# Kernel tuning notes

Measured on AMD Instinct MI355X. Metric: run time of the kernel, lower is better.

Reference implementation:

```python
import jax, jax.numpy as jnp
import numpy as np

B, H, V, T = 32768, 1024, 9, 20
EOS = 8

def setup_inputs() -> dict:
    key = jax.random.key(0)
    ks = jax.random.split(key, 10)
    s_fc = 1.0 / np.sqrt(784)
    s_ih = 1.0 / np.sqrt(V)
    s_hh = 1.0 / np.sqrt(H)
    u = jax.random.uniform(ks[9], (T, B, V), jnp.float32, 1e-10, 1.0)
    return {
        "x": jax.random.normal(ks[0], (B, 784), jnp.float32),
        "tau": jnp.float32(1.0),
        "fc_w": jax.random.normal(ks[1], (H, 784), jnp.float32) * s_fc,
        "w_ih": jax.random.normal(ks[2], (3 * H, V), jnp.float32) * s_ih,
        "w_hh": jax.random.normal(ks[3], (3 * H, H), jnp.float32) * s_hh,
        "b_ih": jax.random.normal(ks[4], (3 * H,), jnp.float32) * s_hh,
        "b_hh": jax.random.normal(ks[5], (3 * H,), jnp.float32) * s_hh,
        "proj_w": jax.random.normal(ks[6], (V, H), jnp.float32) * s_hh,
        "proj_b": jax.random.normal(ks[7], (V,), jnp.float32) * s_hh,
        # standard Gumbel(0,1) noise, precomputed for all T steps
        "gumbel": -jnp.log(-jnp.log(u)),
    }


def reference(x, tau, fc_w, w_ih, w_hh, b_ih, b_hh, proj_w, proj_b, gumbel):
    # context = gelu(fc(x)); dropout is identity (eval mode)
    h0 = jax.nn.gelu(x @ fc_w.T, approximate=False)  # [B, H]
    b = x.shape[0]
    tok0 = jnp.zeros((b, V), x.dtype).at[:, 0].set(1.0)  # BOS one-hot

    def step(carry, g):
        h, tok, finished, lengths, t = carry
        gi = tok @ w_ih.T + b_ih            # [B, 3H]
        gh = h @ w_hh.T + b_hh              # [B, 3H]
        i_r, i_z, i_n = jnp.split(gi, 3, axis=-1)
        h_r, h_z, h_n = jnp.split(gh, 3, axis=-1)
        r = jax.nn.sigmoid(i_r + h_r)
        z = jax.nn.sigmoid(i_z + h_z)
        n = jnp.tanh(i_n + r * h_n)
        h_new = (1.0 - z) * n + z * h
        logits = h_new @ proj_w.T + proj_b  # [B, V]
        y_soft = jax.nn.softmax((logits + g) / tau, axis=-1)
        idx = jnp.argmax(y_soft, axis=-1)
        y_hard = jax.nn.one_hot(idx, V, dtype=y_soft.dtype)
        y = y_hard + y_soft - jax.lax.stop_gradient(y_soft)  # straight-through
        newly = (idx == EOS) & (~finished)
        lengths = jnp.where(newly, t + 1, lengths)
        finished = finished | newly
        return (h_new, y, finished, lengths, t + 1), y

    carry0 = (h0, tok0,
              jnp.zeros((b,), jnp.bool_),
              jnp.full((b,), T, jnp.int32),
              jnp.int32(0))
    (_, _, _, lengths, _), toks = jax.lax.scan(step, carry0, gumbel)
    message = jnp.transpose(toks, (1, 0, 2))  # [B, T, V]
    return message, lengths
```

## Files before the change

### kernel.cpp

```cpp
#include <hip/hip_runtime.h>
#include <math.h>

#define Bsz 32768
#define Hd  1024
#define Vn  9
#define Tn  20
#define EOSv 8
#define KFC 784

typedef float f4 __attribute__((ext_vector_type(4)));
typedef float f32x16 __attribute__((ext_vector_type(16)));
typedef _Float16 h8 __attribute__((ext_vector_type(8)));
typedef unsigned short us4 __attribute__((ext_vector_type(4)));
typedef unsigned short us8v __attribute__((ext_vector_type(8)));

__device__ __forceinline__ unsigned short f16_rne(float x) {
    _Float16 h = (_Float16)x;
    return __builtin_bit_cast(unsigned short, h);
}
__device__ __forceinline__ float f16_val(unsigned short u) {
    return (float)__builtin_bit_cast(_Float16, u);
}
__device__ __forceinline__ void split2h(float x, unsigned short& p0, unsigned short& p1) {
    p0 = f16_rne(x);
    float r = x - f16_val(p0);
    p1 = f16_rne(r);
}

__global__ __launch_bounds__(256) void k_init(int* __restrict__ st,
                                              float* __restrict__ lenf) {
    int i = blockIdx.x * 256 + threadIdx.x;
    if (i < Bsz) { st[i] = 0; lenf[i] = (float)Tn; }
}

__global__ __launch_bounds__(256) void k_prep(const float* __restrict__ wih,
                                              const float* __restrict__ bih,
                                              float* __restrict__ giTab) {
    int i = blockIdx.x * 256 + threadIdx.x;
    int tk = i / 3072, n = i - tk * 3072;
    giTab[i] = wih[(size_t)n * Vn + tk] + bih[n];
}

__global__ __launch_bounds__(256) void k_prepB(const float* __restrict__ whh,
                                               unsigned short* __restrict__ wp) {
    int g = blockIdx.x * 256 + threadIdx.x;
    int lane = g & 63, u = g >> 6;
    int p = u & 1, kc = (u >> 1) & 63, ct = u >> 7;
    int col = ct * 32 + (lane & 31);
    int k = kc * 16 + (lane >> 5) * 8;
    const float* src = whh + (size_t)col * Hd + k;
    unsigned short v[8];
    #pragma unroll
    for (int i = 0; i < 8; ++i) {
        unsigned short s0, s1; split2h(src[i], s0, s1);
        v[i] = (p == 0) ? s0 : s1;
    }
    unsigned short* dst = wp + (size_t)u * 512 + lane * 8;
    us4 w0; w0[0]=v[0]; w0[1]=v[1]; w0[2]=v[2]; w0[3]=v[3];
    us4 w1; w1[0]=v[4]; w1[1]=v[5]; w1[2]=v[6]; w1[3]=v[7];
    *(us4*)dst = w0;
    *(us4*)(dst + 4) = w1;
}

__global__ __launch_bounds__(256) void k_fcP(const float* __restrict__ x,
                                             const float* __restrict__ fcw,
                                             float* __restrict__ h0,
                                             unsigned short* __restrict__ ap) {
    __shared__ float As[16][68];
    __shared__ float Ws[16][68];
    const int tid = threadIdx.x;
    const int tx = tid & 15, ty = tid >> 4;
    const int m0 = blockIdx.x * 64, n0 = blockIdx.y * 64;
    const int lrow = tid >> 2, lkc = (tid & 3) << 2;
    float acc[4][4] = {};
    for (int k0 = 0; k0 < KFC; k0 += 16) {
        f4 a = *(const f4*)(x   + (size_t)(m0 + lrow) * KFC + k0 + lkc);
        f4 w = *(const f4*)(fcw + (size_t)(n0 + lrow) * KFC + k0 + lkc);
        #pragma unroll
        for (int q = 0; q < 4; ++q) { As[lkc + q][lrow] = a[q]; Ws[lkc + q][lrow] = w[q]; }
        __syncthreads();
        #pragma unroll
        for (int kk = 0; kk < 16; ++kk) {
            f4 av = *(const f4*)&As[kk][ty * 4];
            f4 wv = *(const f4*)&Ws[kk][tx * 4];
            #pragma unroll
            for (int i = 0; i < 4; ++i)
                #pragma unroll
                for (int j = 0; j < 4; ++j)
                    acc[i][j] = fmaf(av[i], wv[j], acc[i][j]);
        }
        __syncthreads();
    }
    #pragma unroll
    for (int i = 0; i < 4; ++i) {
        const int row = m0 + ty * 4 + i;
        const int cb = n0 + tx * 4;
        f4 hv;
        us4 q0, q1;
        #pragma unroll
        for (int j = 0; j < 4; ++j) {
            float v = acc[i][j];
            float gl = 0.5f * v * (1.0f + erff(v * 0.70710678118654752f));
            hv[j] = gl;
            unsigned short s0, s1; split2h(gl, s0, s1);
            q0[j] = s0; q1[j] = s1;
        }
        *(f4*)&h0[(size_t)row * Hd + cb] = hv;
        const size_t ub = ((size_t)(row >> 5) * 64 + (cb >> 4)) * 2;
        const int slot = (row & 31) + ((cb >> 3) & 1) * 32;
        const int eo = (tx & 1) * 4;
        *(us4*)&ap[(ub + 0) * 512 + slot * 8 + eo] = q0;
        *(us4*)&ap[(ub + 1) * 512 + slot * 8 + eo] = q1;
    }
}

__global__ __launch_bounds__(256, 2) void k_step(
        const unsigned short* __restrict__ ap, float* __restrict__ h,
        const unsigned short* __restrict__ wp, const float* __restrict__ bhh,
        const float* __restrict__ giTab, const int* __restrict__ st) {
    const int tid = threadIdx.x;
    const int lane = tid & 63, wid = tid >> 6;
    const int wm = wid >> 1, wn = wid & 1;
    const int l31 = lane & 31, lh = lane >> 5;

    const int w = blockIdx.x;
    const int cg = (w & 7) * 2 + ((w >> 3) & 1);
    const int rb = w >> 4;
    const int m_blk = rb * 128;
    const int c0 = cg * 64;

    f32x16 acc[2][3];
    #pragma unroll
    for (int mt = 0; mt < 2; ++mt)
        #pragma unroll
        for (int g = 0; g < 3; ++g)
            #pragma unroll
            for (int e = 0; e < 16; ++e) acc[mt][g][e] = 0.0f;

    const unsigned short* ab[2][2];
    #pragma unroll
    for (int mt = 0; mt < 2; ++mt)
        #pragma unroll
        for (int p = 0; p < 2; ++p)
            ab[mt][p] = ap + ((size_t)(rb * 4 + wm * 2 + mt) * 64 * 2 + p) * 512 + lane * 8;
    const unsigned short* bb[3][2];
    #pragma unroll
    for (int g = 0; g < 3; ++g)
        #pragma unroll
        for (int p = 0; p < 2; ++p)
            bb[g][p] = wp + ((size_t)(g * 32 + cg * 2 + wn) * 64 * 2 + p) * 512 + lane * 8;

    h8 A0[2][2], A1[2][2], B0[3][2], B1[3][2];

    auto load = [&](int s, h8 (&A)[2][2], h8 (&B)[3][2]) {
        const size_t off = (size_t)s * 1024;
        #pragma unroll
        for (int mt = 0; mt < 2; ++mt)
            #pragma unroll
            for (int p = 0; p < 2; ++p)
                A[mt][p] = *(const h8*)(ab[mt][p] + off);
        #pragma unroll
        for (int g = 0; g < 3; ++g)
            #pragma unroll
            for (int p = 0; p < 2; ++p)
                B[g][p] = *(const h8*)(bb[g][p] + off);
    };
    auto compute = [&](h8 (&A)[2][2], h8 (&B)[3][2]) {
        #pragma unroll
        for (int ps = 0; ps < 3; ++ps)
            #pragma unroll
            for (int g = 0; g < 3; ++g)
                #pragma unroll
                for (int mt = 0; mt < 2; ++mt) {
                    h8 a = (ps == 1) ? A[mt][1] : A[mt][0];
                    h8 b = (ps == 0) ? B[g][1] : B[g][0];
                    acc[mt][g] = __builtin_amdgcn_mfma_f32_32x32x16_f16(a, b, acc[mt][g], 0, 0, 0);
                }
    };

    load(0, A0, B0);
    load(1, A1, B1);
    for (int s2 = 0; s2 < 32; ++s2) {
        const int s = s2 * 2;
        compute(A0, B0);
        if (s + 2 < 64) load(s + 2, A0, B0);
        compute(A1, B1);
        if (s + 3 < 64) load(s + 3, A1, B1);
    }

    const int col = c0 + wn * 32 + l31;
    const float bhr = bhh[col], bhz = bhh[Hd + col], bhn = bhh[2 * Hd + col];
    #pragma unroll
    for (int mt = 0; mt < 2; ++mt) {
        #pragma unroll
        for (int reg = 0; reg < 16; ++reg) {
            const int row = m_blk + wm * 64 + mt * 32 + 4 * lh + (reg & 3) + 8 * (reg >> 2);
            const int tk = st[row] & 15;
            const float* gi = giTab + tk * 3072;
            float rr = 1.0f / (1.0f + expf(-(gi[col] + acc[mt][0][reg] + bhr)));
            float zz = 1.0f / (1.0f + expf(-(gi[Hd + col] + acc[mt][1][reg] + bhz)));
            float nn = tanhf(gi[2 * Hd + col] + rr * (acc[mt][2][reg] + bhn));
            const size_t off = (size_t)row * Hd + col;
            float hold = h[off];
            h[off] = (1.0f - zz) * nn + zz * hold;
        }
    }
}

__global__ __launch_bounds__(256) void k_projP(const float* __restrict__ hnew,
        unsigned short* __restrict__ ap,
        const float* __restrict__ pw, const float* __restrict__ pb,
        const float* __restrict__ gum, const float* __restrict__ tau,
        float* __restrict__ msg, float* __restrict__ lenf,
        int* __restrict__ st, int t) {
    const int lane = threadIdx.x & 63;
    const int wv = threadIdx.x >> 6;
    const int b = blockIdx.x * 4 + wv;
    const float* hr = hnew + (size_t)b * Hd;
    float s[Vn] = {};
    float vals[16];
    #pragma unroll
    for (int c0 = 0; c0 < 16; c0 += 4) {
        f4 hv = *(const f4*)(hr + lane * 16 + c0);
        #pragma unroll
        for (int q = 0; q < 4; ++q) vals[c0 + q] = hv[q];
        #pragma unroll
        for (int v = 0; v < Vn; ++v) {
            f4 pv = *(const f4*)(pw + (size_t)v * Hd + lane * 16 + c0);
            #pragma unroll
            for (int q = 0; q < 4; ++q) s[v] = fmaf(hv[q], pv[q], s[v]);
        }
    }
    us8v o0[2], o1[2];
    #pragma unroll
    for (int hh = 0; hh < 2; ++hh)
        #pragma unroll
        for (int e = 0; e < 8; ++e) {
            unsigned short q0, q1;
            split2h(vals[hh * 8 + e], q0, q1);
            o0[hh][e] = q0; o1[hh][e] = q1;
        }
    const size_t ub = ((size_t)(b >> 5) * 64 + lane) * 2;
    const int sl = (b & 31) * 8;
    *(us8v*)&ap[(ub + 0) * 512 + sl]       = o0[0];
    *(us8v*)&ap[(ub + 0) * 512 + sl + 256] = o0[1];
    *(us8v*)&ap[(ub + 1) * 512 + sl]       = o1[0];
    *(us8v*)&ap[(ub + 1) * 512 + sl + 256] = o1[1];
    #pragma unroll
    for (int v = 0; v < Vn; ++v)
        #pragma unroll
        for (int off = 32; off > 0; off >>= 1)
            s[v] += __shfl_xor(s[v], off, 64);
    if (lane == 0) {
        const float tv = tau[0];
        float zv[Vn];
        #pragma unroll
        for (int v = 0; v < Vn; ++v)
            zv[v] = (s[v] + pb[v] + gum[(size_t)b * Vn + v]) / tv;
        int idx = 0; float m = zv[0];
        #pragma unroll
        for (int v = 1; v < Vn; ++v)
            if (zv[v] > m) { m = zv[v]; idx = v; }
        float* orow = msg + ((size_t)b * Tn + t) * Vn;
        #pragma unroll
        for (int v = 0; v < Vn; ++v) orow[v] = (v == idx) ? 1.0f : 0.0f;
        const int old = st[b];
        const int fn = old >> 4;
        st[b] = idx | (((fn != 0) || (idx == EOSv)) ? 16 : 0);
        if (idx == EOSv && fn == 0) lenf[b] = (float)(t + 1);
    }
}

extern "C" void kernel_launch(void* const* d_in, const int* in_sizes, int n_in,
                              void* d_out, int out_size, void* d_ws, size_t ws_size,
                              hipStream_t stream) {
    const float* x   = (const float*)d_in[0];
    const float* tau = (const float*)d_in[1];
    const float* fcw = (const float*)d_in[2];
    const float* wih = (const float*)d_in[3];
    const float* whh = (const float*)d_in[4];
    const float* bih = (const float*)d_in[5];
    const float* bhh = (const float*)d_in[6];
    const float* pw  = (const float*)d_in[7];
    const float* pb  = (const float*)d_in[8];
    const float* gum = (const float*)d_in[9];

    float* msg  = (float*)d_out;
    float* lenf = msg + (size_t)Bsz * Tn * Vn;

    char* ws = (char*)d_ws;
    float*          h     = (float*)ws;
    unsigned short* apb   = (unsigned short*)(ws + 134217728ull);
    unsigned short* wpb   = (unsigned short*)(ws + 268435456ull);
    float*          giTab = (float*)(ws + 281018368ull);
    int*            st    = (int*)  (ws + 281128960ull);

    k_init<<<Bsz / 256, 256, 0, stream>>>(st, lenf);
    k_prep<<<108, 256, 0, stream>>>(wih, bih, giTab);
    k_prepB<<<3072, 256, 0, stream>>>(whh, wpb);
    k_fcP<<<dim3(Bsz / 64, Hd / 64), 256, 0, stream>>>(x, fcw, h, apb);
    for (int t = 0; t < Tn; ++t) {
        k_step<<<4096, 256, 0, stream>>>(apb, h, wpb, bhh, giTab, st);
        k_projP<<<Bsz / 4, 256, 0, stream>>>(h, apb, pw, pb,
                                             gum + (size_t)t * Bsz * Vn,
                                             tau, msg, lenf, st, t);
    }
}
```

Before: 17.98 ms.

## Retile GRU step GEMM to 512x32 blocks with LDS-staged shared weights

Reshapes the recurrent GEMM tile from 128 rows by 64 columns to 512 rows by 32 columns per block. Each wave now owns 128 rows. The W_hh fragments are staged once per block into double-buffered LDS with global_load_lds and shared by all four waves, instead of each wave loading its own B fragments from global memory. This is meant to cut redundant weight traffic and raise arithmetic intensity per block. In exchange, accumulator register pressure doubles, occupancy drops to one block per CU, and each k-step needs explicit vmcnt waits and barriers.

```diff
diff --git a/kernel.cpp b/kernel.cpp
--- a/kernel.cpp
+++ b/kernel.cpp
@@ -26,6 +26,15 @@
     float r = x - f16_val(p0);
     p1 = f16_rne(r);
 }
+
+__device__ __forceinline__ void gload16(const void* g, void* l) {
+    __builtin_amdgcn_global_load_lds(
+        (const __attribute__((address_space(1))) unsigned int*)g,
+        (__attribute__((address_space(3))) unsigned int*)l, 16, 0, 0);
+}
+
+#define V_WAIT(N) asm volatile("s_waitcnt vmcnt(" #N ")" ::: "memory")
+#define BARRIER   asm volatile("s_barrier" ::: "memory")
 
 __global__ __launch_bounds__(256) void k_init(int* __restrict__ st,
                                               float* __restrict__ lenf) {
@@ -114,87 +123,107 @@
     }
 }
 
-__global__ __launch_bounds__(256, 2) void k_step(
+__global__ __launch_bounds__(256, 1) void k_step(
         const unsigned short* __restrict__ ap, float* __restrict__ h,
         const unsigned short* __restrict__ wp, const float* __restrict__ bhh,
         const float* __restrict__ giTab, const int* __restrict__ st) {
+    __shared__ unsigned short Bsm[2][6 * 512];
     const int tid = threadIdx.x;
     const int lane = tid & 63, wid = tid >> 6;
-    const int wm = wid >> 1, wn = wid & 1;
     const int l31 = lane & 31, lh = lane >> 5;
 
     const int w = blockIdx.x;
-    const int cg = (w & 7) * 2 + ((w >> 3) & 1);
-    const int rb = w >> 4;
-    const int m_blk = rb * 128;
-    const int c0 = cg * 64;
-
-    f32x16 acc[2][3];
-    #pragma unroll
-    for (int mt = 0; mt < 2; ++mt)
+    const int cg = (w & 7) * 4 + ((w >> 3) & 3);
+    const int rb = w >> 5;
+    const int m_blk = rb * 512;
+    const int c0 = cg * 32;
+
+    f32x16 acc[4][3];
+    #pragma unroll
+    for (int mt = 0; mt < 4; ++mt)
         #pragma unroll
         for (int g = 0; g < 3; ++g)
             #pragma unroll
             for (int e = 0; e < 16; ++e) acc[mt][g][e] = 0.0f;
 
-    const unsigned short* ab[2][2];
-    #pragma unroll
-    for (int mt = 0; mt < 2; ++mt)
+    const unsigned short* ab[4][2];
+    #pragma unroll
+    for (int mt = 0; mt < 4; ++mt)
         #pragma unroll
         for (int p = 0; p < 2; ++p)
-            ab[mt][p] = ap + ((size_t)(rb * 4 + wm * 2 + mt) * 64 * 2 + p) * 512 + lane * 8;
-    const unsigned short* bb[3][2];
-    #pragma unroll
-    for (int g = 0; g < 3; ++g)
-        #pragma unroll
-        for (int p = 0; p < 2; ++p)
-            bb[g][p] = wp + ((size_t)(g * 32 + cg * 2 + wn) * 64 * 2 + p) * 512 + lane * 8;
-
-    h8 A0[2][2], A1[2][2], B0[3][2], B1[3][2];
-
-    auto load = [&](int s, h8 (&A)[2][2], h8 (&B)[3][2]) {
+            ab[mt][p] = ap + ((size_t)(rb * 16 + wid * 4 + mt) * 64 * 2 + p) * 512 + lane * 8;
+
+    h8 A0[4][2], A1[4][2];
+    auto load_a = [&](int s, h8 (&A)[4][2]) {
         const size_t off = (size_t)s * 1024;
         #pragma unroll
-        for (int mt = 0; mt < 2; ++mt)
+        for (int mt = 0; mt < 4; ++mt)
             #pragma unroll
             for (int p = 0; p < 2; ++p)
                 A[mt][p] = *(const h8*)(ab[mt][p] + off);
+    };
+    auto stage_b = [&](int s, int bufi) {
+        {
+            const int u = wid;
+            const int g = u >> 1, p = u & 1;
+            const unsigned short* src = wp + ((size_t)((g * 32 + cg) * 64 + s) * 2 + p) * 512 + lane * 8;
+            gload16(src, &Bsm[bufi][u * 512]);
+        }
+        if (wid < 2) {
+            const int u = 4 + wid;
+            const int g = u >> 1, p = u & 1;
+            const unsigned short* src = wp + ((size_t)((g * 32 + cg) * 64 + s) * 2 + p) * 512 + lane * 8;
+            gload16(src, &Bsm[bufi][u * 512]);
+        }
+    };
+    auto compute = [&](h8 (&A)[4][2], int bufi) {
+        h8 B[3][2];
         #pragma unroll
         for (int g = 0; g < 3; ++g)
             #pragma unroll
             for (int p = 0; p < 2; ++p)
-                B[g][p] = *(const h8*)(bb[g][p] + off);
-    };
-    auto compute = [&](h8 (&A)[2][2], h8 (&B)[3][2]) {
+                B[g][p] = *(const h8*)&Bsm[bufi][(g * 2 + p) * 512 + lane * 8];
         #pragma unroll
         for (int ps = 0; ps < 3; ++ps)
             #pragma unroll
             for (int g = 0; g < 3; ++g)
                 #pragma unroll
-                for (int mt = 0; mt < 2; ++mt) {
+                for (int mt = 0; mt < 4; ++mt) {
                     h8 a = (ps == 1) ? A[mt][1] : A[mt][0];
                     h8 b = (ps == 0) ? B[g][1] : B[g][0];
                     acc[mt][g] = __builtin_amdgcn_mfma_f32_32x32x16_f16(a, b, acc[mt][g], 0, 0, 0);
                 }
     };
 
-    load(0, A0, B0);
-    load(1, A1, B1);
+    stage_b(0, 0);
+    load_a(0, A0);
+    load_a(1, A1);
+    V_WAIT(8);
+    BARRIER;
+
     for (int s2 = 0; s2 < 32; ++s2) {
         const int s = s2 * 2;
-        compute(A0, B0);
-        if (s + 2 < 64) load(s + 2, A0, B0);
-        compute(A1, B1);
-        if (s + 3 < 64) load(s + 3, A1, B1);
-    }
-
-    const int col = c0 + wn * 32 + l31;
+        stage_b(s + 1, 1);
+        compute(A0, 0);
+        if (s + 2 < 64) load_a(s + 2, A0);
+        if (s2 < 31) { V_WAIT(8); } else { V_WAIT(0); }
+        BARRIER;
+        if (s + 2 < 64) stage_b(s + 2, 0);
+        compute(A1, 1);
+        if (s + 3 < 64) load_a(s + 3, A1);
+        if (s2 < 31) {
+            if (s2 < 30) { V_WAIT(8); } else { V_WAIT(0); }
+            BARRIER;
+        }
+    }
+
+    const int col = c0 + l31;
     const float bhr = bhh[col], bhz = bhh[Hd + col], bhn = bhh[2 * Hd + col];
     #pragma unroll
-    for (int mt = 0; mt < 2; ++mt) {
+    for (int mt = 0; mt < 4; ++mt) {
         #pragma unroll
         for (int reg = 0; reg < 16; ++reg) {
-            const int row = m_blk + wm * 64 + mt * 32 + 4 * lh + (reg & 3) + 8 * (reg >> 2);
+            const int row = m_blk + wid * 128 + mt * 32 + 4 * lh + (reg & 3) + 8 * (reg >> 2);
             const int tk = st[row] & 15;
             const float* gi = giTab + tk * 3072;
             float rr = 1.0f / (1.0f + expf(-(gi[col] + acc[mt][0][reg] + bhr)));
@@ -300,7 +329,7 @@
     k_prepB<<<3072, 256, 0, stream>>>(whh, wpb);
     k_fcP<<<dim3(Bsz / 64, Hd / 64), 256, 0, stream>>>(x, fcw, h, apb);
     for (int t = 0; t < Tn; ++t) {
-        k_step<<<4096, 256, 0, stream>>>(apb, h, wpb, bhh, giTab, st);
+        k_step<<<2048, 256, 0, stream>>>(apb, h, wpb, bhh, giTab, st);
         k_projP<<<Bsz / 4, 256, 0, stream>>>(h, apb, pw, pb,
                                              gum + (size_t)t * Bsz * Vn,
                                              tau, msg, lenf, st, t);
```

Result: slower. 21.53 ms (+19.8%).

## Stage GRU step GEMM tiles through LDS with async loads and triple buffering

Applied to the files above, without the earlier changes.

The recurrent step kernel now uses 512-thread blocks that cover 256 rows instead of 128, so each weight tile is shared by more rows. A and B fragments are copied into a three-deep LDS ring with global_load_lds, replacing per-wave register prefetch from global memory, and stages are synchronised with vmcnt waits and barriers. The aim is to halve redundant weight traffic and overlap loads with MFMA work, at the cost of about 84KB of LDS per block, which may limit occupancy, plus a barrier on every k-step.

```diff
diff --git a/kernel.cpp b/kernel.cpp
--- a/kernel.cpp
+++ b/kernel.cpp
@@ -26,6 +26,15 @@
     float r = x - f16_val(p0);
     p1 = f16_rne(r);
 }
+
+__device__ __forceinline__ void gload16(const void* g, void* l) {
+    __builtin_amdgcn_global_load_lds(
+        (const __attribute__((address_space(1))) unsigned int*)g,
+        (__attribute__((address_space(3))) unsigned int*)l, 16, 0, 0);
+}
+
+#define V_WAIT(N) asm volatile("s_waitcnt vmcnt(" #N ")" ::: "memory")
+#define BARRIER   asm volatile("s_barrier" ::: "memory")
 
 __global__ __launch_bounds__(256) void k_init(int* __restrict__ st,
                                               float* __restrict__ lenf) {
@@ -114,10 +123,11 @@
     }
 }
 
-__global__ __launch_bounds__(256, 2) void k_step(
+__global__ __launch_bounds__(512, 2) void k_step(
         const unsigned short* __restrict__ ap, float* __restrict__ h,
         const unsigned short* __restrict__ wp, const float* __restrict__ bhh,
         const float* __restrict__ giTab, const int* __restrict__ st) {
+    __shared__ unsigned short Sm[3][28 * 512];
     const int tid = threadIdx.x;
     const int lane = tid & 63, wid = tid >> 6;
     const int wm = wid >> 1, wn = wid & 1;
@@ -126,7 +136,7 @@
     const int w = blockIdx.x;
     const int cg = (w & 7) * 2 + ((w >> 3) & 1);
     const int rb = w >> 4;
-    const int m_blk = rb * 128;
+    const int m_blk = rb * 256;
     const int c0 = cg * 64;
 
     f32x16 acc[2][3];
@@ -137,55 +147,65 @@
             #pragma unroll
             for (int e = 0; e < 16; ++e) acc[mt][g][e] = 0.0f;
 
-    const unsigned short* ab[2][2];
-    #pragma unroll
-    for (int mt = 0; mt < 2; ++mt)
-        #pragma unroll
-        for (int p = 0; p < 2; ++p)
-            ab[mt][p] = ap + ((size_t)(rb * 4 + wm * 2 + mt) * 64 * 2 + p) * 512 + lane * 8;
-    const unsigned short* bb[3][2];
-    #pragma unroll
-    for (int g = 0; g < 3; ++g)
-        #pragma unroll
-        for (int p = 0; p < 2; ++p)
-            bb[g][p] = wp + ((size_t)(g * 32 + cg * 2 + wn) * 64 * 2 + p) * 512 + lane * 8;
-
-    h8 A0[2][2], A1[2][2], B0[3][2], B1[3][2];
-
-    auto load = [&](int s, h8 (&A)[2][2], h8 (&B)[3][2]) {
-        const size_t off = (size_t)s * 1024;
+    auto stage = [&](int s, int bi) {
+        if (wid < 4) {
+            #pragma unroll
+            for (int j = 0; j < 4; ++j) {
+                const int u = wid * 4 + j;
+                const int rg = rb * 8 + (u >> 1), p = u & 1;
+                const unsigned short* src = ap + ((size_t)(rg * 64 + s) * 2 + p) * 512 + lane * 8;
+                gload16(src, &Sm[bi][u * 512]);
+            }
+        } else {
+            #pragma unroll
+            for (int j = 0; j < 3; ++j) {
+                const int b = (wid - 4) * 3 + j;
+                const int wnl = b / 6, rem = b - wnl * 6;
+                const int g = rem >> 1, p = rem & 1;
+                const int ct = g * 32 + cg * 2 + wnl;
+                const unsigned short* src = wp + ((size_t)(ct * 64 + s) * 2 + p) * 512 + lane * 8;
+                gload16(src, &Sm[bi][(16 + b) * 512]);
+            }
+        }
+    };
+    auto compute = [&](int bi) {
+        h8 af[2][2], bf[3][2];
         #pragma unroll
         for (int mt = 0; mt < 2; ++mt)
             #pragma unroll
             for (int p = 0; p < 2; ++p)
-                A[mt][p] = *(const h8*)(ab[mt][p] + off);
+                af[mt][p] = *(const h8*)&Sm[bi][(((wm * 2 + mt) * 2 + p)) * 512 + lane * 8];
         #pragma unroll
         for (int g = 0; g < 3; ++g)
             #pragma unroll
             for (int p = 0; p < 2; ++p)
-                B[g][p] = *(const h8*)(bb[g][p] + off);
-    };
-    auto compute = [&](h8 (&A)[2][2], h8 (&B)[3][2]) {
+                bf[g][p] = *(const h8*)&Sm[bi][(16 + wn * 6 + g * 2 + p) * 512 + lane * 8];
         #pragma unroll
         for (int ps = 0; ps < 3; ++ps)
             #pragma unroll
             for (int g = 0; g < 3; ++g)
                 #pragma unroll
                 for (int mt = 0; mt < 2; ++mt) {
-                    h8 a = (ps == 1) ? A[mt][1] : A[mt][0];
-                    h8 b = (ps == 0) ? B[g][1] : B[g][0];
+                    h8 a = (ps == 1) ? af[mt][1] : af[mt][0];
+                    h8 b = (ps == 0) ? bf[g][1] : bf[g][0];
                     acc[mt][g] = __builtin_amdgcn_mfma_f32_32x32x16_f16(a, b, acc[mt][g], 0, 0, 0);
                 }
     };
 
-    load(0, A0, B0);
-    load(1, A1, B1);
-    for (int s2 = 0; s2 < 32; ++s2) {
-        const int s = s2 * 2;
-        compute(A0, B0);
-        if (s + 2 < 64) load(s + 2, A0, B0);
-        compute(A1, B1);
-        if (s + 3 < 64) load(s + 3, A1, B1);
+    stage(0, 0);
+    stage(1, 1);
+    if (wid < 4) { V_WAIT(4); } else { V_WAIT(3); }
+    BARRIER;
+
+    for (int s = 0; s < 64; ++s) {
+        const int bi = s % 3;
+        if (s < 62) stage(s + 2, (s + 2) % 3);
+        compute(bi);
+        if (s < 63) {
+            if (s < 62) { if (wid < 4) { V_WAIT(4); } else { V_WAIT(3); } }
+            else        { V_WAIT(0); }
+            BARRIER;
+        }
     }
 
     const int col = c0 + wn * 32 + l31;
@@ -300,7 +320,7 @@
     k_prepB<<<3072, 256, 0, stream>>>(whh, wpb);
     k_fcP<<<dim3(Bsz / 64, Hd / 64), 256, 0, stream>>>(x, fcw, h, apb);
     for (int t = 0; t < Tn; ++t) {
-        k_step<<<4096, 256, 0, stream>>>(apb, h, wpb, bhh, giTab, st);
+        k_step<<<2048, 512, 0, stream>>>(apb, h, wpb, bhh, giTab, st);
         k_projP<<<Bsz / 4, 256, 0, stream>>>(h, apb, pw, pb,
                                              gum + (size_t)t * Bsz * Vn,
                                              tau, msg, lenf, st, t);
```

After: 17.93 ms. Within noise of the previous version (-0.3%).
